# Performance work log

Hardware: AMD Instinct MI355X
Metric: run time of the kernel (lower is better)

## Reference

```python
import jax, jax.numpy as jnp
import numpy as np

SPATIAL_SHAPES = [(160, 160), (80, 80), (40, 40)]
D_MODEL = 256
N_HEADS = 8
N_LEVELS = 3
N_POINTS = 4
B = 1
SEQ = sum(h * w for h, w in SPATIAL_SHAPES)  # 33600


def setup_inputs() -> dict:
    key = jax.random.key(0)
    ks = jax.random.split(key, 10)
    f = jax.random.normal
    return {
        "hidden_states": f(ks[0], (B, SEQ, D_MODEL), jnp.float32),
        "encoder_hidden_states": f(ks[1], (B, SEQ, D_MODEL), jnp.float32),
        "position_embeddings": f(ks[2], (B, SEQ, D_MODEL), jnp.float32),
        "reference_points": jax.random.uniform(ks[3], (B, SEQ, N_LEVELS, 2), jnp.float32),
        "Wv": f(ks[4], (D_MODEL, D_MODEL), jnp.float32) * 0.02,
        "bv": jnp.zeros((D_MODEL,), jnp.float32),
        "Ws": f(ks[5], (N_HEADS * N_LEVELS * N_POINTS * 2, D_MODEL), jnp.float32) * 0.02,
        "bs": f(ks[6], (N_HEADS * N_LEVELS * N_POINTS * 2,), jnp.float32) * 2.0,
        "Wa": f(ks[7], (N_HEADS * N_LEVELS * N_POINTS, D_MODEL), jnp.float32) * 0.02,
        "ba": jnp.zeros((N_HEADS * N_LEVELS * N_POINTS,), jnp.float32),
        "Wo": f(ks[8], (D_MODEL, D_MODEL), jnp.float32) * 0.02,
        "bo": jnp.zeros((D_MODEL,), jnp.float32),
    }


def grid_sample_bilinear(img, grid):
    """torch.nn.functional.grid_sample, mode='bilinear', padding_mode='zeros', align_corners=False.
    img: [N, C, Hi, Wi]; grid: [N, Hg, Wg, 2] with (x, y) in [-1, 1]. Returns [N, C, Hg, Wg]."""
    N, C, Hi, Wi = img.shape
    x = (grid[..., 0] + 1.0) * (Wi * 0.5) - 0.5  # unnormalized pixel coords
    y = (grid[..., 1] + 1.0) * (Hi * 0.5) - 0.5
    x0f = jnp.floor(x)
    y0f = jnp.floor(y)
    x0 = x0f.astype(jnp.int32)
    y0 = y0f.astype(jnp.int32)
    wx1 = x - x0f
    wy1 = y - y0f
    imgc = jnp.transpose(img, (0, 2, 3, 1))  # [N, Hi, Wi, C]
    n_idx = jnp.arange(N)[:, None, None]

    def tap(xi, yi, w):
        valid = (xi >= 0) & (xi < Wi) & (yi >= 0) & (yi < Hi)
        xc = jnp.clip(xi, 0, Wi - 1)
        yc = jnp.clip(yi, 0, Hi - 1)
        v = imgc[n_idx, yc, xc]  # [N, Hg, Wg, C]
        return v * (w * valid.astype(img.dtype))[..., None]

    out = (tap(x0, y0, (1.0 - wx1) * (1.0 - wy1))
           + tap(x0 + 1, y0, wx1 * (1.0 - wy1))
           + tap(x0, y0 + 1, (1.0 - wx1) * wy1)
           + tap(x0 + 1, y0 + 1, wx1 * wy1))
    return jnp.transpose(out, (0, 3, 1, 2))  # [N, C, Hg, Wg]


def reference(hidden_states, encoder_hidden_states, position_embeddings, reference_points,
              Wv, bv, Ws, bs, Wa, ba, Wo, bo):
    hd = D_MODEL // N_HEADS
    LP = N_LEVELS * N_POINTS
    Q = SEQ

    hs = hidden_states + position_embeddings  # [B, Q, D]
    value = (encoder_hidden_states @ Wv.T + bv).reshape(B, SEQ, N_HEADS, hd)
    offsets = (hs @ Ws.T + bs).reshape(B * Q, N_HEADS, LP, 2)
    attn = jax.nn.softmax((hs @ Wa.T + ba).reshape(B, Q, N_HEADS, LP), axis=-1)

    # offset normalizer: [w, h] per level, broadcast over points
    norm = jnp.array([[w, h] for (h, w) in SPATIAL_SHAPES], jnp.float32)  # [L, 2]
    norm = jnp.broadcast_to(norm[:, None, :], (N_LEVELS, N_POINTS, 2)).reshape(1, 1, LP, 2)
    rp = reference_points.reshape(-1, N_LEVELS, 1, 2)
    rp = jnp.broadcast_to(rp, (B * Q, N_LEVELS, N_POINTS, 2)).reshape(B * Q, 1, LP, 2)
    loc = rp + offsets / norm                # [BQ, H, LP, 2]
    grids = 2.0 * loc - 1.0

    attn_t = jnp.transpose(attn, (0, 2, 1, 3)).reshape(B * N_HEADS, 1, Q, LP)

    sampled = []
    start = 0
    for lvl, (h, w) in enumerate(SPATIAL_SHAPES):
        v = value[:, start:start + h * w].reshape(B, h * w, N_HEADS * hd)
        v = jnp.transpose(v, (0, 2, 1)).reshape(B * N_HEADS, hd, h, w)
        g = jnp.transpose(grids[:, :, lvl * N_POINTS:(lvl + 1) * N_POINTS], (1, 0, 2, 3))  # [H, BQ, P, 2] (B=1)
        sampled.append(grid_sample_bilinear(v, g))  # [B*H, hd, Q, P]
        start += h * w

    out = (jnp.concatenate(sampled, axis=-1) * attn_t).sum(-1)  # [B*H, hd, Q]
    out = jnp.transpose(out.reshape(B, N_HEADS * hd, Q), (0, 2, 1))  # [B, Q, D]
    output = out @ Wo.T + bo
    return output, attn
```

## Files before the change

### kernel.cpp

```cpp
#include <hip/hip_runtime.h>
#include <math.h>

#define QSEQ 33600

typedef __attribute__((ext_vector_type(8))) short short8;
typedef __attribute__((ext_vector_type(4))) float floatx4;
typedef unsigned short ushort_t;

static __device__ __forceinline__ ushort_t f2bf(float f) {
  unsigned u = __float_as_uint(f);
  return (ushort_t)((u + 0x7FFF + ((u >> 16) & 1)) >> 16);
}

static __device__ __forceinline__ void gload_lds16(const void* g, void* l) {
  __builtin_amdgcn_global_load_lds((__attribute__((address_space(1))) void*)g,
                                   (__attribute__((address_space(3))) void*)l, 16, 0, 0);
}

template <int ASRC, int MODE>
static __device__ __forceinline__ void gemm_body(
    const int bx, const int by,
    const float* __restrict__ A1, const float* __restrict__ A2,
    const ushort_t* __restrict__ Ab,
    const float* __restrict__ B1, const float* __restrict__ B2, const int bsplit,
    const float* __restrict__ b1, const float* __restrict__ b2,
    void* __restrict__ C1, float* __restrict__ C2, const int N,
    ushort_t* smem) {
  ushort_t* As = smem;
  ushort_t* Bs = smem + 6144;

  const int tid = threadIdx.x;
  const int m0 = by * 96;
  const int n0 = bx * 128;
  const int wv = tid >> 6, lane = tid & 63;
  const int wm = wv >> 1, wn = wv & 1;
  const int l16 = lane & 15, quad = lane >> 4;
  const int l8 = l16 & 7;

  const float* gAf[3];
  const float* gAf2[3];
  const ushort_t* gAb[3];
  ushort_t* lA[3];
#pragma unroll
  for (int i = 0; i < 3; ++i) {
    const int c = tid + i * 256;
    const int row = c >> 3, s = c & 7;
    if (ASRC == 0) {
      gAb[i] = Ab + (size_t)(m0 + row) * 256 + ((s ^ (row & 7)) * 8);
      lA[i] = As + (wv * 64 + i * 256) * 8;
    } else {
      gAf[i] = A1 + (size_t)(m0 + row) * 256 + s * 8;
      if (ASRC == 2) gAf2[i] = A2 + (size_t)(m0 + row) * 256 + s * 8;
      lA[i] = As + row * 64 + (s ^ (row & 7)) * 8;
    }
  }
  const float* gBf[4];
  ushort_t* lBf[4];
#pragma unroll
  for (int j = 0; j < 4; ++j) {
    const int c = tid + j * 256;
    const int row = c >> 3, s = c & 7;
    const int grow = n0 + row;
    const float* bsrc;
    int r2;
    if (grow < bsplit) {
      bsrc = B1;
      r2 = grow;
    } else {
      bsrc = B2;
      r2 = grow - bsplit;
      const int rmax = N - bsplit - 1;
      if (r2 > rmax) r2 = rmax;
    }
    gBf[j] = bsrc + (size_t)r2 * 256 + s * 8;
    lBf[j] = Bs + row * 64 + (s ^ (row & 7)) * 8;
  }

  floatx4 acc[3][4];
#pragma unroll
  for (int i = 0; i < 3; ++i)
#pragma unroll
    for (int j = 0; j < 4; ++j) acc[i][j] = (floatx4)(0.f);

  for (int k0 = 0; k0 < 256; k0 += 64) {
    if (ASRC == 0) {
#pragma unroll
      for (int i = 0; i < 3; ++i) gload_lds16(gAb[i] + k0, lA[i]);
    } else {
#pragma unroll
      for (int i = 0; i < 3; ++i) {
        const float4 x0 = *(const float4*)(gAf[i] + k0);
        const float4 x1 = *(const float4*)(gAf[i] + k0 + 4);
        float v[8] = {x0.x, x0.y, x0.z, x0.w, x1.x, x1.y, x1.z, x1.w};
        if (ASRC == 2) {
          const float4 y0 = *(const float4*)(gAf2[i] + k0);
          const float4 y1 = *(const float4*)(gAf2[i] + k0 + 4);
          v[0] += y0.x; v[1] += y0.y; v[2] += y0.z; v[3] += y0.w;
          v[4] += y1.x; v[5] += y1.y; v[6] += y1.z; v[7] += y1.w;
        }
        ushort_t t[8];
#pragma unroll
        for (int e = 0; e < 8; ++e) t[e] = f2bf(v[e]);
        *(short8*)lA[i] = *(const short8*)t;
      }
    }
#pragma unroll
    for (int j = 0; j < 4; ++j) {
      const float4 x0 = *(const float4*)(gBf[j] + k0);
      const float4 x1 = *(const float4*)(gBf[j] + k0 + 4);
      ushort_t t[8] = {f2bf(x0.x), f2bf(x0.y), f2bf(x0.z), f2bf(x0.w),
                       f2bf(x1.x), f2bf(x1.y), f2bf(x1.z), f2bf(x1.w)};
      *(short8*)lBf[j] = *(const short8*)t;
    }
    __syncthreads();

#pragma unroll
    for (int k32 = 0; k32 < 2; ++k32) {
      const int cx = ((k32 * 4 + quad) ^ l8) * 8;
      short8 a[3], b[4];
#pragma unroll
      for (int mi = 0; mi < 3; ++mi)
        a[mi] = *(const short8*)&As[(wm * 48 + mi * 16 + l16) * 64 + cx];
#pragma unroll
      for (int ni = 0; ni < 4; ++ni)
        b[ni] = *(const short8*)&Bs[(wn * 64 + ni * 16 + l16) * 64 + cx];
#pragma unroll
      for (int mi = 0; mi < 3; ++mi)
#pragma unroll
        for (int ni = 0; ni < 4; ++ni)
          acc[mi][ni] = __builtin_amdgcn_mfma_f32_16x16x32_bf16(a[mi], b[ni], acc[mi][ni], 0, 0, 0);
    }
    __syncthreads();
  }

  if (MODE == 0) {
    float* C = (float*)C1;
#pragma unroll
    for (int ni = 0; ni < 4; ++ni) {
      const int col = n0 + wn * 64 + ni * 16 + l16;
      const float bia = b1[col];
#pragma unroll
      for (int mi = 0; mi < 3; ++mi) {
        const int rr = m0 + wm * 48 + mi * 16 + quad * 4;
#pragma unroll
        for (int r = 0; r < 4; ++r)
          C[(size_t)(rr + r) * N + col] = acc[mi][ni][r] + bia;
      }
    }
  } else if (MODE == 1) {
    ushort_t* C = (ushort_t*)C1;
#pragma unroll
    for (int ni = 0; ni < 4; ++ni) {
      const int col = n0 + wn * 64 + ni * 16 + l16;
      const float bia = b1[col];
      const int h = col >> 5, ch = col & 31;
#pragma unroll
      for (int mi = 0; mi < 3; ++mi) {
        const int rr = m0 + wm * 48 + mi * 16 + quad * 4;
#pragma unroll
        for (int r = 0; r < 4; ++r)
          C[((size_t)h * QSEQ + rr + r) * 32 + ch] = f2bf(acc[mi][ni][r] + bia);
      }
    }
  } else {
    float* smf = (float*)smem;
#pragma unroll
    for (int ni = 0; ni < 4; ++ni) {
      const int col = n0 + wn * 64 + ni * 16 + l16;
      if (col < 96) {
        const float bia = b1[col];
#pragma unroll
        for (int mi = 0; mi < 3; ++mi) {
          const int lr = wm * 48 + mi * 16 + quad * 4;
#pragma unroll
          for (int r = 0; r < 4; ++r)
            smf[(lr + r) * 96 + col] = acc[mi][ni][r] + bia;
        }
      } else if (col < 288) {
        const float bia = b2[col - 96];
#pragma unroll
        for (int mi = 0; mi < 3; ++mi) {
          const int rr = m0 + wm * 48 + mi * 16 + quad * 4;
#pragma unroll
          for (int r = 0; r < 4; ++r)
            C2[(size_t)(rr + r) * 192 + (col - 96)] = acc[mi][ni][r] + bia;
        }
      }
    }
    __syncthreads();
    if (bx == 0) {
      float* C = (float*)C1;
#pragma unroll
      for (int p = 0; p < 3; ++p) {
        const int task = tid + p * 256;
        const int row = task >> 3, hh = task & 7;
        float v[12];
        float mx = -1e30f;
#pragma unroll
        for (int i = 0; i < 12; ++i) {
          v[i] = smf[row * 96 + hh * 12 + i];
          mx = fmaxf(mx, v[i]);
        }
        float s = 0.f;
#pragma unroll
        for (int i = 0; i < 12; ++i) {
          v[i] = __expf(v[i] - mx);
          s += v[i];
        }
        const float inv = 1.f / s;
        float4 o[3];
#pragma unroll
        for (int i = 0; i < 3; ++i) {
          o[i].x = v[i * 4 + 0] * inv;
          o[i].y = v[i * 4 + 1] * inv;
          o[i].z = v[i * 4 + 2] * inv;
          o[i].w = v[i * 4 + 3] * inv;
        }
        float4* dst = (float4*)&C[(size_t)(m0 + row) * 96 + hh * 12];
        dst[0] = o[0];
        dst[1] = o[1];
        dst[2] = o[2];
      }
    }
  }
}

__global__ __launch_bounds__(256) void pre_gemms(
    const float* __restrict__ ehs, const float* __restrict__ hidden,
    const float* __restrict__ pos,
    const float* __restrict__ Wv, const float* __restrict__ bv,
    const float* __restrict__ Wa, const float* __restrict__ ba,
    const float* __restrict__ Ws, const float* __restrict__ bs,
    ushort_t* __restrict__ value, float* __restrict__ attn,
    float* __restrict__ sp) {
  extern __shared__ ushort_t smem[];
  if (blockIdx.x < 2)
    gemm_body<1, 1>(blockIdx.x, blockIdx.y, ehs, nullptr, nullptr,
                    Wv, Wv, 1 << 30, bv, nullptr, value, nullptr, 256, smem);
  else
    gemm_body<2, 2>(blockIdx.x - 2, blockIdx.y, hidden, pos, nullptr,
                    Wa, Ws, 96, ba, bs, attn, sp, 288, smem);
}

__global__ __launch_bounds__(256) void out_gemm(
    const ushort_t* __restrict__ samp, const float* __restrict__ Wo,
    const float* __restrict__ bo, float* __restrict__ out) {
  extern __shared__ ushort_t smem[];
  gemm_body<0, 0>(blockIdx.x, blockIdx.y, nullptr, nullptr, samp,
                  Wo, Wo, 1 << 30, bo, nullptr, out, nullptr, 256, smem);
}

__global__ __launch_bounds__(256) void msda_sample_kernel(
    const ushort_t* __restrict__ value,
    const float* __restrict__ sp,
    const float* __restrict__ attn,
    const float* __restrict__ refp,
    ushort_t* __restrict__ outp) {
  const int h = blockIdx.x & 7;
  const int q = (blockIdx.x >> 3) * 4 + (threadIdx.x >> 6);
  const int lane = threadIdx.x & 63;
  const int cg = lane >> 4, pt = lane & 15;
  const int ptc = pt < 12 ? pt : 11;
  const int lvl = ptc >> 2;
  const int S = lvl == 0 ? 160 : (lvl == 1 ? 80 : 40);
  const int base = lvl == 0 ? 0 : (lvl == 1 ? 25600 : 32000);

  float a = attn[q * 96 + h * 12 + ptc];
  a = pt < 12 ? a : 0.f;
  const float2 off = *(const float2*)&sp[q * 192 + h * 24 + ptc * 2];
  const float2 rp = *(const float2*)&refp[q * 6 + lvl * 2];

  const float x = fmaf(rp.x, (float)S, off.x) - 0.5f;
  const float y = fmaf(rp.y, (float)S, off.y) - 0.5f;
  const float xf = floorf(x), yf = floorf(y);
  const int x0 = (int)xf, y0 = (int)yf;
  const float wx1 = x - xf, wy1 = y - yf;

  const float wx0z = (x0 >= 0 && x0 < S) ? 1.f - wx1 : 0.f;
  const float wx1z = (x0 + 1 >= 0 && x0 + 1 < S) ? wx1 : 0.f;
  const float wy0z = (y0 >= 0 && y0 < S) ? 1.f - wy1 : 0.f;
  const float wy1z = (y0 + 1 >= 0 && y0 + 1 < S) ? wy1 : 0.f;

  const int x0c = min(max(x0, 0), S - 1);
  const int x1c = min(max(x0 + 1, 0), S - 1);
  const int y0c = min(max(y0, 0), S - 1);
  const int y1c = min(max(y0 + 1, 0), S - 1);

  const float w00 = a * wx0z * wy0z, w10 = a * wx1z * wy0z;
  const float w01 = a * wx0z * wy1z, w11 = a * wx1z * wy1z;

  const ushort_t* hb = value + ((h * QSEQ + base) << 5) + cg * 8;
  const int r0 = y0c * S, r1 = y1c * S;
  const uint4 u00 = *(const uint4*)(hb + ((r0 + x0c) << 5));
  const uint4 u10 = *(const uint4*)(hb + ((r0 + x1c) << 5));
  const uint4 u01 = *(const uint4*)(hb + ((r1 + x0c) << 5));
  const uint4 u11 = *(const uint4*)(hb + ((r1 + x1c) << 5));

  float facc[8];
  {
    const unsigned a0[4] = {u00.x, u00.y, u00.z, u00.w};
    const unsigned a1[4] = {u10.x, u10.y, u10.z, u10.w};
    const unsigned a2[4] = {u01.x, u01.y, u01.z, u01.w};
    const unsigned a3[4] = {u11.x, u11.y, u11.z, u11.w};
#pragma unroll
    for (int i = 0; i < 4; ++i) {
      float lo = __uint_as_float(a0[i] << 16) * w00;
      float hi = __uint_as_float(a0[i] & 0xFFFF0000u) * w00;
      lo = fmaf(__uint_as_float(a1[i] << 16), w10, lo);
      hi = fmaf(__uint_as_float(a1[i] & 0xFFFF0000u), w10, hi);
      lo = fmaf(__uint_as_float(a2[i] << 16), w01, lo);
      hi = fmaf(__uint_as_float(a2[i] & 0xFFFF0000u), w01, hi);
      lo = fmaf(__uint_as_float(a3[i] << 16), w11, lo);
      hi = fmaf(__uint_as_float(a3[i] & 0xFFFF0000u), w11, hi);
      facc[2 * i + 0] = lo;
      facc[2 * i + 1] = hi;
    }
  }

#pragma unroll
  for (int m = 1; m < 16; m <<= 1)
#pragma unroll
    for (int i = 0; i < 8; ++i) facc[i] += __shfl_xor(facc[i], m, 64);

  if (pt == 0) {
    ushort_t t[8];
#pragma unroll
    for (int i = 0; i < 8; ++i) t[i] = f2bf(facc[i]);
    *(uint4*)&outp[(size_t)q * 256 + h * 32 + cg * 8] = *(const uint4*)t;
  }
}

extern "C" void kernel_launch(void* const* d_in, const int* in_sizes, int n_in,
                              void* d_out, int out_size, void* d_ws, size_t ws_size,
                              hipStream_t stream) {
  const float* hidden = (const float*)d_in[0];
  const float* ehs    = (const float*)d_in[1];
  const float* pos    = (const float*)d_in[2];
  const float* refp   = (const float*)d_in[3];
  const float* Wv = (const float*)d_in[4];
  const float* bv = (const float*)d_in[5];
  const float* Ws = (const float*)d_in[6];
  const float* bs = (const float*)d_in[7];
  const float* Wa = (const float*)d_in[8];
  const float* ba = (const float*)d_in[9];
  const float* Wo = (const float*)d_in[10];
  const float* bo = (const float*)d_in[11];

  float* out  = (float*)d_out;
  float* attn = out + (size_t)QSEQ * 256;

  char* ws = (char*)d_ws;
  ushort_t* ws_value = (ushort_t*)ws;
  ushort_t* ws_outp  = ws_value + (size_t)QSEQ * 256;
  float* ws_sp = (float*)(ws_outp + (size_t)QSEQ * 256);

  dim3 blk(256);

  pre_gemms<<<dim3(5, 350), blk, 36864, stream>>>(
      ehs, hidden, pos, Wv, bv, Wa, ba, Ws, bs, ws_value, attn, ws_sp);
  msda_sample_kernel<<<dim3((QSEQ / 4) * 8), blk, 0, stream>>>(
      ws_value, ws_sp, attn, refp, ws_outp);
  out_gemm<<<dim3(2, 350), blk, 28672, stream>>>(ws_outp, Wo, bo, out);
}
```

Measured before the change: 296.2 us.

## Restructure MSDA sampling with LDS weight/offset table and per-channel accumulation

The sampling kernel now handles 4 queries and all 8 heads per block. It first computes the bilinear weights and byte offsets for every (query, head, point) into a shared-memory table. Each thread then owns 4 channels of one head and loops over all 48 taps, accumulating directly in registers. This removes the 16-lane cross-lane shuffle reduction and the 4 wasted padding lanes, at the cost of a barrier, extra LDS traffic and narrower 8-byte gathers.

```diff
diff --git a/kernel.cpp b/kernel.cpp
--- a/kernel.cpp
+++ b/kernel.cpp
@@ -256,78 +256,80 @@
     const float* __restrict__ attn,
     const float* __restrict__ refp,
     ushort_t* __restrict__ outp) {
-  const int h = blockIdx.x & 7;
-  const int q = (blockIdx.x >> 3) * 4 + (threadIdx.x >> 6);
-  const int lane = threadIdx.x & 63;
-  const int cg = lane >> 4, pt = lane & 15;
-  const int ptc = pt < 12 ? pt : 11;
-  const int lvl = ptc >> 2;
-  const int S = lvl == 0 ? 160 : (lvl == 1 ? 80 : 40);
-  const int base = lvl == 0 ? 0 : (lvl == 1 ? 25600 : 32000);
-
-  float a = attn[q * 96 + h * 12 + ptc];
-  a = pt < 12 ? a : 0.f;
-  const float2 off = *(const float2*)&sp[q * 192 + h * 24 + ptc * 2];
-  const float2 rp = *(const float2*)&refp[q * 6 + lvl * 2];
-
-  const float x = fmaf(rp.x, (float)S, off.x) - 0.5f;
-  const float y = fmaf(rp.y, (float)S, off.y) - 0.5f;
-  const float xf = floorf(x), yf = floorf(y);
-  const int x0 = (int)xf, y0 = (int)yf;
-  const float wx1 = x - xf, wy1 = y - yf;
-
-  const float wx0z = (x0 >= 0 && x0 < S) ? 1.f - wx1 : 0.f;
-  const float wx1z = (x0 + 1 >= 0 && x0 + 1 < S) ? wx1 : 0.f;
-  const float wy0z = (y0 >= 0 && y0 < S) ? 1.f - wy1 : 0.f;
-  const float wy1z = (y0 + 1 >= 0 && y0 + 1 < S) ? wy1 : 0.f;
-
-  const int x0c = min(max(x0, 0), S - 1);
-  const int x1c = min(max(x0 + 1, 0), S - 1);
-  const int y0c = min(max(y0, 0), S - 1);
-  const int y1c = min(max(y0 + 1, 0), S - 1);
-
-  const float w00 = a * wx0z * wy0z, w10 = a * wx1z * wy0z;
-  const float w01 = a * wx0z * wy1z, w11 = a * wx1z * wy1z;
-
-  const ushort_t* hb = value + ((h * QSEQ + base) << 5) + cg * 8;
-  const int r0 = y0c * S, r1 = y1c * S;
-  const uint4 u00 = *(const uint4*)(hb + ((r0 + x0c) << 5));
-  const uint4 u10 = *(const uint4*)(hb + ((r0 + x1c) << 5));
-  const uint4 u01 = *(const uint4*)(hb + ((r1 + x0c) << 5));
-  const uint4 u11 = *(const uint4*)(hb + ((r1 + x1c) << 5));
-
-  float facc[8];
-  {
-    const unsigned a0[4] = {u00.x, u00.y, u00.z, u00.w};
-    const unsigned a1[4] = {u10.x, u10.y, u10.z, u10.w};
-    const unsigned a2[4] = {u01.x, u01.y, u01.z, u01.w};
-    const unsigned a3[4] = {u11.x, u11.y, u11.z, u11.w};
-#pragma unroll
-    for (int i = 0; i < 4; ++i) {
-      float lo = __uint_as_float(a0[i] << 16) * w00;
-      float hi = __uint_as_float(a0[i] & 0xFFFF0000u) * w00;
-      lo = fmaf(__uint_as_float(a1[i] << 16), w10, lo);
-      hi = fmaf(__uint_as_float(a1[i] & 0xFFFF0000u), w10, hi);
-      lo = fmaf(__uint_as_float(a2[i] << 16), w01, lo);
-      hi = fmaf(__uint_as_float(a2[i] & 0xFFFF0000u), w01, hi);
-      lo = fmaf(__uint_as_float(a3[i] << 16), w11, lo);
-      hi = fmaf(__uint_as_float(a3[i] & 0xFFFF0000u), w11, hi);
-      facc[2 * i + 0] = lo;
-      facc[2 * i + 1] = hi;
-    }
-  }
-
-#pragma unroll
-  for (int m = 1; m < 16; m <<= 1)
-#pragma unroll
-    for (int i = 0; i < 8; ++i) facc[i] += __shfl_xor(facc[i], m, 64);
-
-  if (pt == 0) {
-    ushort_t t[8];
-#pragma unroll
-    for (int i = 0; i < 8; ++i) t[i] = f2bf(facc[i]);
-    *(uint4*)&outp[(size_t)q * 256 + h * 32 + cg * 8] = *(const uint4*)t;
-  }
+  __shared__ unsigned wtab[32 * 100];
+  const int tid = threadIdx.x;
+  const int qbase = blockIdx.x * 4;
+
+#pragma unroll
+  for (int pass = 0; pass < 2; ++pass) {
+    const int it = tid + pass * 256;
+    if (it < 384) {
+      const int task = it / 12;
+      const int pt = it - task * 12;
+      const int q = qbase + (task >> 3);
+      const int h = task & 7;
+      const int lvl = pt >> 2;
+      const int S = lvl == 0 ? 160 : (lvl == 1 ? 80 : 40);
+      const int base = lvl == 0 ? 0 : (lvl == 1 ? 25600 : 32000);
+
+      const float a = attn[q * 96 + h * 12 + pt];
+      const float2 off = *(const float2*)&sp[q * 192 + h * 24 + pt * 2];
+      const float2 rp = *(const float2*)&refp[q * 6 + lvl * 2];
+
+      const float x = fmaf(rp.x, (float)S, off.x) - 0.5f;
+      const float y = fmaf(rp.y, (float)S, off.y) - 0.5f;
+      const float xf = floorf(x), yf = floorf(y);
+      const int x0 = (int)xf, y0 = (int)yf;
+      const float wx1 = x - xf, wy1 = y - yf;
+
+      const float wx0z = (x0 >= 0 && x0 < S) ? 1.f - wx1 : 0.f;
+      const float wx1z = (x0 + 1 >= 0 && x0 + 1 < S) ? wx1 : 0.f;
+      const float wy0z = (y0 >= 0 && y0 < S) ? 1.f - wy1 : 0.f;
+      const float wy1z = (y0 + 1 >= 0 && y0 + 1 < S) ? wy1 : 0.f;
+
+      const int x0c = min(max(x0, 0), S - 1);
+      const int x1c = min(max(x0 + 1, 0), S - 1);
+      const int y0c = min(max(y0, 0), S - 1);
+      const int y1c = min(max(y0 + 1, 0), S - 1);
+
+      const int r0 = base + y0c * S, r1 = base + y1c * S;
+      uint4 e0, e1;
+      e0.x = __float_as_uint(a * wx0z * wy0z);
+      e0.y = (unsigned)(r0 + x0c) << 6;
+      e0.z = __float_as_uint(a * wx1z * wy0z);
+      e0.w = (unsigned)(r0 + x1c) << 6;
+      e1.x = __float_as_uint(a * wx0z * wy1z);
+      e1.y = (unsigned)(r1 + x0c) << 6;
+      e1.z = __float_as_uint(a * wx1z * wy1z);
+      e1.w = (unsigned)(r1 + x1c) << 6;
+      unsigned* dst = &wtab[task * 100 + pt * 8];
+      *(uint4*)dst = e0;
+      *(uint4*)(dst + 4) = e1;
+    }
+  }
+  __syncthreads();
+
+  const int wv = tid >> 6;
+  const int h = (tid >> 3) & 7;
+  const int c = tid & 7;
+  const int q = qbase + wv;
+  const unsigned* wt = &wtab[(wv * 8 + h) * 100];
+  const char* vbase = (const char*)value + ((size_t)h * QSEQ) * 64 + c * 8;
+
+  float f0 = 0.f, f1 = 0.f, f2 = 0.f, f3 = 0.f;
+#pragma unroll
+  for (int r = 0; r < 48; ++r) {
+    const uint2 e = *(const uint2*)&wt[r * 2];
+    const float w = __uint_as_float(e.x);
+    const uint2 v = *(const uint2*)(vbase + e.y);
+    f0 = fmaf(__uint_as_float(v.x << 16), w, f0);
+    f1 = fmaf(__uint_as_float(v.x & 0xFFFF0000u), w, f1);
+    f2 = fmaf(__uint_as_float(v.y << 16), w, f2);
+    f3 = fmaf(__uint_as_float(v.y & 0xFFFF0000u), w, f3);
+  }
+
+  ushort_t t[4] = {f2bf(f0), f2bf(f1), f2bf(f2), f2bf(f3)};
+  *(uint2*)&outp[(size_t)q * 256 + h * 32 + c * 4] = *(const uint2*)t;
 }
 
 extern "C" void kernel_launch(void* const* d_in, const int* in_sizes, int n_in,
@@ -358,7 +360,7 @@
 
   pre_gemms<<<dim3(5, 350), blk, 36864, stream>>>(
       ehs, hidden, pos, Wv, bv, Wa, ba, Ws, bs, ws_value, attn, ws_sp);
-  msda_sample_kernel<<<dim3((QSEQ / 4) * 8), blk, 0, stream>>>(
+  msda_sample_kernel<<<dim3(QSEQ / 4), blk, 0, stream>>>(
       ws_value, ws_sp, attn, refp, ws_outp);
   out_gemm<<<dim3(2, 350), blk, 28672, stream>>>(ws_outp, Wo, bo, out);
 }
```

Measured after the change: 288.8 us. 2.5% less time.
